# Optimization experiments

Hardware: AMD Instinct MI355X
Metric: run time of the kernel (lower is better)

Reference implementation:

```python
import jax, jax.numpy as jnp
import numpy as np

N_NODES = 100000
N_EDGES = 1600000
NFEAT = 512
HIDDEN = 128
NCLASS = 40


def setup_inputs() -> dict:
    key = jax.random.key(0)
    ks = jax.random.split(key, 8)
    x = jax.random.normal(ks[0], (N_NODES, NFEAT), dtype=jnp.float32)
    edge_src = jax.random.randint(ks[1], (N_EDGES,), 0, N_NODES, dtype=jnp.int32)
    edge_dst = jax.random.randint(ks[2], (N_EDGES,), 0, N_NODES, dtype=jnp.int32)
    # normalized adjacency values (D^-1/2 A D^-1/2 style), all positive
    edge_val = jax.random.uniform(ks[3], (N_EDGES,), dtype=jnp.float32)
    # glorot-ish init like pygcn's reset_parameters
    W1 = jax.random.normal(ks[4], (NFEAT, HIDDEN), dtype=jnp.float32) / np.sqrt(NFEAT)
    b1 = jnp.zeros((HIDDEN,), dtype=jnp.float32)
    W2 = jax.random.normal(ks[5], (HIDDEN, NCLASS), dtype=jnp.float32) / np.sqrt(HIDDEN)
    b2 = jnp.zeros((NCLASS,), dtype=jnp.float32)
    return {"x": x, "edge_src": edge_src, "edge_dst": edge_dst, "edge_val": edge_val,
            "W1": W1, "b1": b1, "W2": W2, "b2": b2}


def _gcn_layer(h, edge_src, edge_dst, edge_val, W, b):
    # support = h @ W ; out = spmm(adj, support) + b
    support = h @ W                                  # [N, d_out]
    msg = support[edge_src] * edge_val[:, None]      # [E, d_out] gather
    agg = jax.ops.segment_sum(msg, edge_dst, num_segments=N_NODES)  # scatter-add
    return agg + b


def reference(x, edge_src, edge_dst, edge_val, W1, b1, W2, b2):
    h = _gcn_layer(x, edge_src, edge_dst, edge_val, W1, b1)
    h = jax.nn.relu(h)
    # dropout=0.0 -> branch skipped (faithful to `if self.dropout:` with falsy value)
    h = _gcn_layer(h, edge_src, edge_dst, edge_val, W2, b2)
    return jax.nn.log_softmax(h, axis=1)
```

## Files before the change

kernel.cpp:

```cpp
#include <hip/hip_runtime.h>
#include <stdint.h>

#define NN 100000
#define NE 1600000
#define NF 512
#define NH 128
#define NC 40

typedef float f32x4 __attribute__((ext_vector_type(4)));
typedef short bf16x8 __attribute__((ext_vector_type(8)));

__device__ __forceinline__ unsigned short f2bf(float f){
    unsigned u = __float_as_uint(f);
    u = u + 0x7FFFu + ((u >> 16) & 1u);
    return (unsigned short)(u >> 16);
}
__device__ __forceinline__ unsigned pk2(float a, float b){
    return (unsigned)f2bf(a) | ((unsigned)f2bf(b) << 16);
}
__device__ __forceinline__ float bf2f(unsigned short s){
    return __uint_as_float(((unsigned)s) << 16);
}
__device__ __forceinline__ float blo(unsigned u){ return __uint_as_float(u << 16); }
__device__ __forceinline__ float bhi(unsigned u){ return __uint_as_float(u & 0xffff0000u); }

__global__ __launch_bounds__(256) void hist_prep(const int* __restrict__ edst,
                       int* __restrict__ deg, int* __restrict__ posw,
                       const float* __restrict__ W1, const float* __restrict__ W2,
                       unsigned short* __restrict__ W1t, unsigned short* __restrict__ W2t){
    if (blockIdx.x < 280){
        int tid = blockIdx.x * 256 + threadIdx.x;
        if (tid < NF * NH){
            int c = tid >> 9;
            int k = tid & 511;
            W1t[c * NF + k] = f2bf(W1[k * NH + c]);
        }
        int t2 = tid - NF * NH;
        if (t2 >= 0 && t2 < 48 * NH){
            int c = t2 >> 7;
            int k = t2 & 127;
            W2t[c * NH + k] = (c < NC) ? f2bf(W2[k * NC + c]) : (unsigned short)0;
        }
    } else {
        int tid = (blockIdx.x - 280) * 256 + threadIdx.x;
        if (tid < NE){
            int d = edst[tid];
            posw[tid] = atomicAdd(&deg[d], 1);
        }
    }
}

__global__ __launch_bounds__(256, 3) void gemm1(const float* __restrict__ x,
                                                const unsigned short* __restrict__ W1t,
                                                unsigned short* __restrict__ s1){
    __shared__ unsigned short Al[2][128 * 40];
    __shared__ unsigned short Bl[2][128 * 40];
    const int tid  = threadIdx.x;
    const int wid  = tid >> 6;
    const int lane = tid & 63;
    const int quad = lane >> 4;
    const int l15  = lane & 15;
    const int br   = blockIdx.x * 128;

    const int r    = tid >> 1;
    const int half = tid & 1;

    int arow = br + r; if (arow >= NN) arow = NN - 1;
    const float* aptr = x + (size_t)arow * NF + half * 16;
    const unsigned short* bptr = W1t + (size_t)r * NF + half * 16;

    float4 pa0, pa1, pa2, pa3;
    uint4  pb0, pb1;
    {
        const float4* ap = (const float4*)aptr;
        pa0 = ap[0]; pa1 = ap[1]; pa2 = ap[2]; pa3 = ap[3];
        const uint4* bp = (const uint4*)bptr;
        pb0 = bp[0]; pb1 = bp[1];
        unsigned* Ad = (unsigned*)&Al[0][r * 40 + half * 16];
        Ad[0] = pk2(pa0.x, pa0.y); Ad[1] = pk2(pa0.z, pa0.w);
        Ad[2] = pk2(pa1.x, pa1.y); Ad[3] = pk2(pa1.z, pa1.w);
        Ad[4] = pk2(pa2.x, pa2.y); Ad[5] = pk2(pa2.z, pa2.w);
        Ad[6] = pk2(pa3.x, pa3.y); Ad[7] = pk2(pa3.z, pa3.w);
        uint4* Bd = (uint4*)&Bl[0][r * 40 + half * 16];
        Bd[0] = pb0; Bd[1] = pb1;
    }
    __syncthreads();

    f32x4 acc[2][8];
#pragma unroll
    for (int i = 0; i < 2; i++)
#pragma unroll
        for (int j = 0; j < 8; j++) acc[i][j] = (f32x4){0.f, 0.f, 0.f, 0.f};

    int cur = 0;
    for (int ks = 0; ks < NF; ks += 32){
        const bool more = (ks + 32 < NF);
        if (more){
            const float4* ap = (const float4*)(aptr + ks + 32);
            pa0 = ap[0]; pa1 = ap[1]; pa2 = ap[2]; pa3 = ap[3];
            const uint4* bp = (const uint4*)(bptr + ks + 32);
            pb0 = bp[0]; pb1 = bp[1];
        }

        bf16x8 a0 = *(const bf16x8*)&Al[cur][(wid * 32 +      l15) * 40 + quad * 8];
        bf16x8 a1 = *(const bf16x8*)&Al[cur][(wid * 32 + 16 + l15) * 40 + quad * 8];
        bf16x8 bb[8];
#pragma unroll
        for (int ct = 0; ct < 8; ct++)
            bb[ct] = *(const bf16x8*)&Bl[cur][(ct * 16 + l15) * 40 + quad * 8];
#pragma unroll
        for (int ct = 0; ct < 8; ct++){
            acc[0][ct] = __builtin_amdgcn_mfma_f32_16x16x32_bf16(a0, bb[ct], acc[0][ct], 0, 0, 0);
            acc[1][ct] = __builtin_amdgcn_mfma_f32_16x16x32_bf16(a1, bb[ct], acc[1][ct], 0, 0, 0);
        }

        if (more){
            int nxt = cur ^ 1;
            unsigned* Ad = (unsigned*)&Al[nxt][r * 40 + half * 16];
            Ad[0] = pk2(pa0.x, pa0.y); Ad[1] = pk2(pa0.z, pa0.w);
            Ad[2] = pk2(pa1.x, pa1.y); Ad[3] = pk2(pa1.z, pa1.w);
            Ad[4] = pk2(pa2.x, pa2.y); Ad[5] = pk2(pa2.z, pa2.w);
            Ad[6] = pk2(pa3.x, pa3.y); Ad[7] = pk2(pa3.z, pa3.w);
            uint4* Bd = (uint4*)&Bl[nxt][r * 40 + half * 16];
            Bd[0] = pb0; Bd[1] = pb1;
        }
        __syncthreads();
        cur ^= 1;
    }

#pragma unroll
    for (int rt = 0; rt < 2; rt++)
#pragma unroll
        for (int ct = 0; ct < 8; ct++)
#pragma unroll
            for (int i = 0; i < 4; i++){
                int row = br + wid * 32 + rt * 16 + quad * 4 + i;
                if (row < NN) s1[(size_t)row * NH + ct * 16 + l15] = f2bf(acc[rt][ct][i]);
            }
}

__global__ void scan1(const int* __restrict__ deg, int* __restrict__ rs, int* __restrict__ bsums){
    __shared__ int sh[256];
    int t = threadIdx.x;
    int base = blockIdx.x * 1024 + t * 4;
    int v0 = (base     < NN) ? deg[base]     : 0;
    int v1 = (base + 1 < NN) ? deg[base + 1] : 0;
    int v2 = (base + 2 < NN) ? deg[base + 2] : 0;
    int v3 = (base + 3 < NN) ? deg[base + 3] : 0;
    int ssum = v0 + v1 + v2 + v3;
    sh[t] = ssum;
    __syncthreads();
    for (int o = 1; o < 256; o <<= 1){
        int tmp = (t >= o) ? sh[t - o] : 0;
        __syncthreads();
        sh[t] += tmp;
        __syncthreads();
    }
    int excl = sh[t] - ssum;
    if (base     < NN) rs[base]     = excl; excl += v0;
    if (base + 1 < NN) rs[base + 1] = excl; excl += v1;
    if (base + 2 < NN) rs[base + 2] = excl; excl += v2;
    if (base + 3 < NN) rs[base + 3] = excl;
    if (t == 255) bsums[blockIdx.x] = sh[255];
}

__global__ void scan3(int* __restrict__ rs, const int* __restrict__ bsums){
    __shared__ int add_s;
    int t = threadIdx.x;
    if (t < 64){
        int v = 0;
        if (t      < blockIdx.x) v  = bsums[t];
        if (t + 64 < blockIdx.x) v += bsums[t + 64];
#pragma unroll
        for (int o = 32; o; o >>= 1) v += __shfl_xor(v, o, 64);
        if (t == 0) add_s = v;
    }
    __syncthreads();
    int add = add_s;
    int base = blockIdx.x * 1024 + t * 4;
#pragma unroll
    for (int i = 0; i < 4; i++)
        if (base + i < NN) rs[base + i] += add;
}

__global__ __launch_bounds__(256) void scatter_k(const int* __restrict__ esrc, const int* __restrict__ edst,
                          const float* __restrict__ eval, const int* __restrict__ rs,
                          const int* __restrict__ posw, int2* __restrict__ pk){
    int tid = blockIdx.x * 256 + threadIdx.x;
    if (tid < NE){
        int d = edst[tid];
        int pos = rs[d] + posw[tid];
        pk[pos] = make_int2(esrc[tid], __float_as_int(eval[tid]));
    }
}

__global__ __launch_bounds__(256) void agg1(const uint2* __restrict__ s1v,
                                            const int* __restrict__ rs,
                                            const int2* __restrict__ pk,
                                            const float* __restrict__ b1, uint2* __restrict__ h){
    const int lane  = threadIdx.x & 63;
    const int half  = lane >> 5;
    const int hl    = lane & 31;
    const int lbase = half * 32;
    const int node  = blockIdx.x * 8 + (threadIdx.x >> 6) * 2 + half;

    int s = rs[node];
    int e = (node == NN - 1) ? NE : rs[node + 1];
    float a0 = 0.f, a1 = 0.f, a2 = 0.f, a3 = 0.f;

    for (int base = s; base < e; base += 32){
        int cnt = e - base; if (cnt > 32) cnt = 32;
        int2 rec = make_int2(0, 0);
        if (hl < cnt) rec = pk[base + hl];
        int j = 0;
        for (; j + 8 <= cnt; j += 8){
            int is[8];
#pragma unroll
            for (int q = 0; q < 8; q++) is[q] = __shfl(rec.x, lbase + j + q, 64);
            uint2 us[8];
#pragma unroll
            for (int q = 0; q < 8; q++) us[q] = s1v[(size_t)is[q] * 32 + hl];
            float vs[8];
#pragma unroll
            for (int q = 0; q < 8; q++) vs[q] = __int_as_float(__shfl(rec.y, lbase + j + q, 64));
#pragma unroll
            for (int q = 0; q < 8; q++){
                a0 += vs[q] * blo(us[q].x); a1 += vs[q] * bhi(us[q].x);
                a2 += vs[q] * blo(us[q].y); a3 += vs[q] * bhi(us[q].y);
            }
        }
        for (; j < cnt; j++){
            int   i0 = __shfl(rec.x, lbase + j, 64);
            float v0 = __int_as_float(__shfl(rec.y, lbase + j, 64));
            uint2 u  = s1v[(size_t)i0 * 32 + hl];
            a0 += v0 * blo(u.x); a1 += v0 * bhi(u.x);
            a2 += v0 * blo(u.y); a3 += v0 * bhi(u.y);
        }
    }
    a0 += b1[4 * hl];     a1 += b1[4 * hl + 1];
    a2 += b1[4 * hl + 2]; a3 += b1[4 * hl + 3];
    a0 = fmaxf(a0, 0.f); a1 = fmaxf(a1, 0.f);
    a2 = fmaxf(a2, 0.f); a3 = fmaxf(a3, 0.f);
    h[(size_t)node * 32 + hl] = make_uint2(pk2(a0, a1), pk2(a2, a3));
}

__global__ __launch_bounds__(256) void gemm2(const unsigned short* __restrict__ h,
                                             const unsigned short* __restrict__ W2t,
                                             unsigned short* __restrict__ s2p){
    const int tid  = threadIdx.x;
    const int wid  = tid >> 6;
    const int lane = tid & 63;
    const int quad = lane >> 4;
    const int l15  = lane & 15;
    const int row0 = blockIdx.x * 64 + wid * 16;

    bf16x8 bf[3][4];
#pragma unroll
    for (int ct = 0; ct < 3; ct++)
#pragma unroll
        for (int ks = 0; ks < 4; ks++)
            bf[ct][ks] = *(const bf16x8*)&W2t[(ct * 16 + l15) * NH + ks * 32 + quad * 8];

    int arow = row0 + l15; if (arow >= NN) arow = NN - 1;
    const unsigned short* ap = h + (size_t)arow * NH;

    bf16x8 a[4];
#pragma unroll
    for (int ks = 0; ks < 4; ks++) a[ks] = *(const bf16x8*)&ap[ks * 32 + quad * 8];

    f32x4 acc[3];
#pragma unroll
    for (int ct = 0; ct < 3; ct++) acc[ct] = (f32x4){0.f, 0.f, 0.f, 0.f};
#pragma unroll
    for (int ks = 0; ks < 4; ks++)
#pragma unroll
        for (int ct = 0; ct < 3; ct++)
            acc[ct] = __builtin_amdgcn_mfma_f32_16x16x32_bf16(a[ks], bf[ct][ks], acc[ct], 0, 0, 0);

#pragma unroll
    for (int ct = 0; ct < 3; ct++)
#pragma unroll
        for (int i = 0; i < 4; i++){
            int row = row0 + quad * 4 + i;
            if (row < NN) s2p[(size_t)row * 64 + ct * 16 + l15] = f2bf(acc[ct][i]);
        }
}

__global__ __launch_bounds__(256) void agg2(const unsigned* __restrict__ s2v,
                                            const int* __restrict__ rs,
                                            const int2* __restrict__ pk,
                                            const float* __restrict__ b2, float* __restrict__ out){
    const int lane  = threadIdx.x & 63;
    const int half  = lane >> 5;
    const int hl    = lane & 31;
    const int lbase = half * 32;
    const int node  = blockIdx.x * 8 + (threadIdx.x >> 6) * 2 + half;

    int s = rs[node];
    int e = (node == NN - 1) ? NE : rs[node + 1];
    float a0 = 0.f, a1 = 0.f;

    for (int base = s; base < e; base += 32){
        int cnt = e - base; if (cnt > 32) cnt = 32;
        int2 rec = make_int2(0, 0);
        if (hl < cnt) rec = pk[base + hl];
        int j = 0;
        for (; j + 8 <= cnt; j += 8){
            int is[8];
#pragma unroll
            for (int q = 0; q < 8; q++) is[q] = __shfl(rec.x, lbase + j + q, 64);
            unsigned us[8];
#pragma unroll
            for (int q = 0; q < 8; q++) us[q] = s2v[(size_t)is[q] * 32 + hl];
            float vs[8];
#pragma unroll
            for (int q = 0; q < 8; q++) vs[q] = __int_as_float(__shfl(rec.y, lbase + j + q, 64));
#pragma unroll
            for (int q = 0; q < 8; q++){
                a0 += vs[q] * blo(us[q]); a1 += vs[q] * bhi(us[q]);
            }
        }
        for (; j < cnt; j++){
            int   i0 = __shfl(rec.x, lbase + j, 64);
            float v0 = __int_as_float(__shfl(rec.y, lbase + j, 64));
            unsigned u = s2v[(size_t)i0 * 32 + hl];
            a0 += v0 * blo(u); a1 += v0 * bhi(u);
        }
    }
    bool act = hl < 20;
    float z0 = act ? (a0 + b2[2 * hl])     : -INFINITY;
    float z1 = act ? (a1 + b2[2 * hl + 1]) : -INFINITY;
    float m = fmaxf(z0, z1);
#pragma unroll
    for (int o = 16; o; o >>= 1) m = fmaxf(m, __shfl_xor(m, o, 64));
    float pe = act ? (__expf(z0 - m) + __expf(z1 - m)) : 0.f;
#pragma unroll
    for (int o = 16; o; o >>= 1) pe += __shfl_xor(pe, o, 64);
    if (act){
        float l = __logf(pe);
        float2 o2 = make_float2(z0 - m - l, z1 - m - l);
        *(float2*)(out + (size_t)node * NC + 2 * hl) = o2;
    }
}

extern "C" void kernel_launch(void* const* d_in, const int* in_sizes, int n_in,
                              void* d_out, int out_size, void* d_ws, size_t ws_size,
                              hipStream_t stream) {
    const float* x    = (const float*)d_in[0];
    const int*   esrc = (const int*)  d_in[1];
    const int*   edst = (const int*)  d_in[2];
    const float* eval = (const float*)d_in[3];
    const float* W1   = (const float*)d_in[4];
    const float* b1   = (const float*)d_in[5];
    const float* W2   = (const float*)d_in[6];
    const float* b2   = (const float*)d_in[7];
    float* out = (float*)d_out;

    char* ws = (char*)d_ws;
    size_t off = 0;
    auto alloc = [&](size_t bytes) -> void* {
        void* p = ws + off;
        off += (bytes + 255) & ~(size_t)255;
        return p;
    };
    unsigned short* W1t  = (unsigned short*)alloc((size_t)NF * NH * 2);
    unsigned short* W2t  = (unsigned short*)alloc((size_t)48 * NH * 2);
    unsigned short* s1   = (unsigned short*)alloc((size_t)NN * NH * 2);
    unsigned short* h    = (unsigned short*)alloc((size_t)NN * NH * 2);
    unsigned short* s2p  = (unsigned short*)alloc((size_t)NN * 64 * 2);
    int*   deg   = (int*)  alloc((size_t)NN * 4);
    int*   rs    = (int*)  alloc((size_t)NN * 4);
    int*   bsums = (int*)  alloc(128 * 4);
    int*   posw  = (int*)  alloc((size_t)NE * 4);
    int2*  pk    = (int2*) alloc((size_t)NE * 8);

    hipMemsetAsync(deg, 0, (size_t)NN * 4, stream);

    hist_prep<<<280 + (NE + 255) / 256, 256, 0, stream>>>(edst, deg, posw, W1, W2, W1t, W2t);
    gemm1    <<<(NN + 127) / 128, 256, 0, stream>>>(x, W1t, s1);
    scan1    <<<98, 256, 0, stream>>>(deg, rs, bsums);
    scan3    <<<98, 256, 0, stream>>>(rs, bsums);
    scatter_k<<<(NE + 255) / 256, 256, 0, stream>>>(esrc, edst, eval, rs, posw, pk);
    agg1     <<<NN / 8, 256, 0, stream>>>((const uint2*)s1, rs, pk, b1, (uint2*)h);
    gemm2    <<<(NN + 63) / 64, 256, 0, stream>>>(h, W2t, s2p);
    agg2     <<<NN / 8, 256, 0, stream>>>((const unsigned*)s2p, rs, pk, b2, out);
}
```

Before: 553.7 us.

## Widen SpMM gathers to 16-byte loads and pack more nodes per wavefront

```diff
diff --git a/kernel.cpp b/kernel.cpp
--- a/kernel.cpp
+++ b/kernel.cpp
@@ -17,9 +17,6 @@
 }
 __device__ __forceinline__ unsigned pk2(float a, float b){
     return (unsigned)f2bf(a) | ((unsigned)f2bf(b) << 16);
-}
-__device__ __forceinline__ float bf2f(unsigned short s){
-    return __uint_as_float(((unsigned)s) << 16);
 }
 __device__ __forceinline__ float blo(unsigned u){ return __uint_as_float(u << 16); }
 __device__ __forceinline__ float bhi(unsigned u){ return __uint_as_float(u & 0xffff0000u); }
@@ -194,54 +191,74 @@
     }
 }
 
-__global__ __launch_bounds__(256) void agg1(const uint2* __restrict__ s1v,
+__global__ __launch_bounds__(256) void agg1(const uint4* __restrict__ s1v,
                                             const int* __restrict__ rs,
                                             const int2* __restrict__ pk,
-                                            const float* __restrict__ b1, uint2* __restrict__ h){
+                                            const float* __restrict__ b1, uint4* __restrict__ h){
     const int lane  = threadIdx.x & 63;
-    const int half  = lane >> 5;
-    const int hl    = lane & 31;
-    const int lbase = half * 32;
-    const int node  = blockIdx.x * 8 + (threadIdx.x >> 6) * 2 + half;
-
-    int s = rs[node];
-    int e = (node == NN - 1) ? NE : rs[node + 1];
-    float a0 = 0.f, a1 = 0.f, a2 = 0.f, a3 = 0.f;
-
-    for (int base = s; base < e; base += 32){
-        int cnt = e - base; if (cnt > 32) cnt = 32;
-        int2 rec = make_int2(0, 0);
-        if (hl < cnt) rec = pk[base + hl];
+    const int quad  = lane >> 4;
+    const int hl    = lane & 15;
+    const int lbase = quad * 16;
+    const int node  = blockIdx.x * 16 + (threadIdx.x >> 6) * 4 + quad;
+
+    const int s = rs[node];
+    const int e = (node == NN - 1) ? NE : rs[node + 1];
+    float a[8];
+#pragma unroll
+    for (int t = 0; t < 8; t++) a[t] = 0.f;
+
+    int2 rec = make_int2(0, 0);
+    {
+        int c0 = e - s; if (c0 > 16) c0 = 16;
+        if (hl < c0) rec = pk[s + hl];
+    }
+    for (int base = s; base < e; base += 16){
+        int cnt = e - base; if (cnt > 16) cnt = 16;
+        int2 cur = rec;
+        int nb = base + 16;
+        if (nb < e){
+            int cn = e - nb; if (cn > 16) cn = 16;
+            rec = make_int2(0, 0);
+            if (hl < cn) rec = pk[nb + hl];
+        }
         int j = 0;
         for (; j + 8 <= cnt; j += 8){
             int is[8];
 #pragma unroll
-            for (int q = 0; q < 8; q++) is[q] = __shfl(rec.x, lbase + j + q, 64);
-            uint2 us[8];
-#pragma unroll
-            for (int q = 0; q < 8; q++) us[q] = s1v[(size_t)is[q] * 32 + hl];
+            for (int q = 0; q < 8; q++) is[q] = __shfl(cur.x, lbase + j + q, 64);
+            uint4 us[8];
+#pragma unroll
+            for (int q = 0; q < 8; q++) us[q] = s1v[(size_t)is[q] * 16 + hl];
             float vs[8];
 #pragma unroll
-            for (int q = 0; q < 8; q++) vs[q] = __int_as_float(__shfl(rec.y, lbase + j + q, 64));
+            for (int q = 0; q < 8; q++) vs[q] = __int_as_float(__shfl(cur.y, lbase + j + q, 64));
 #pragma unroll
             for (int q = 0; q < 8; q++){
-                a0 += vs[q] * blo(us[q].x); a1 += vs[q] * bhi(us[q].x);
-                a2 += vs[q] * blo(us[q].y); a3 += vs[q] * bhi(us[q].y);
+                float v = vs[q];
+                a[0] += v * blo(us[q].x); a[1] += v * bhi(us[q].x);
+                a[2] += v * blo(us[q].y); a[3] += v * bhi(us[q].y);
+                a[4] += v * blo(us[q].z); a[5] += v * bhi(us[q].z);
+                a[6] += v * blo(us[q].w); a[7] += v * bhi(us[q].w);
             }
         }
         for (; j < cnt; j++){
-            int   i0 = __shfl(rec.x, lbase + j, 64);
-            float v0 = __int_as_float(__shfl(rec.y, lbase + j, 64));
-            uint2 u  = s1v[(size_t)i0 * 32 + hl];
-            a0 += v0 * blo(u.x); a1 += v0 * bhi(u.x);
-            a2 += v0 * blo(u.y); a3 += v0 * bhi(u.y);
-        }
-    }
-    a0 += b1[4 * hl];     a1 += b1[4 * hl + 1];
-    a2 += b1[4 * hl + 2]; a3 += b1[4 * hl + 3];
-    a0 = fmaxf(a0, 0.f); a1 = fmaxf(a1, 0.f);
-    a2 = fmaxf(a2, 0.f); a3 = fmaxf(a3, 0.f);
-    h[(size_t)node * 32 + hl] = make_uint2(pk2(a0, a1), pk2(a2, a3));
+            int   i0 = __shfl(cur.x, lbase + j, 64);
+            float v0 = __int_as_float(__shfl(cur.y, lbase + j, 64));
+            uint4 u  = s1v[(size_t)i0 * 16 + hl];
+            a[0] += v0 * blo(u.x); a[1] += v0 * bhi(u.x);
+            a[2] += v0 * blo(u.y); a[3] += v0 * bhi(u.y);
+            a[4] += v0 * blo(u.z); a[5] += v0 * bhi(u.z);
+            a[6] += v0 * blo(u.w); a[7] += v0 * bhi(u.w);
+        }
+    }
+    const float4* b1v = (const float4*)b1;
+    float4 bA = b1v[2 * hl], bB = b1v[2 * hl + 1];
+    a[0] += bA.x; a[1] += bA.y; a[2] += bA.z; a[3] += bA.w;
+    a[4] += bB.x; a[5] += bB.y; a[6] += bB.z; a[7] += bB.w;
+#pragma unroll
+    for (int t = 0; t < 8; t++) a[t] = fmaxf(a[t], 0.f);
+    h[(size_t)node * 16 + hl] = make_uint4(pk2(a[0], a[1]), pk2(a[2], a[3]),
+                                           pk2(a[4], a[5]), pk2(a[6], a[7]));
 }
 
 __global__ __launch_bounds__(256) void gemm2(const unsigned short* __restrict__ h,
@@ -286,60 +303,94 @@
         }
 }
 
-__global__ __launch_bounds__(256) void agg2(const unsigned* __restrict__ s2v,
+__global__ __launch_bounds__(256) void agg2(const uint4* __restrict__ s2v,
                                             const int* __restrict__ rs,
                                             const int2* __restrict__ pk,
                                             const float* __restrict__ b2, float* __restrict__ out){
     const int lane  = threadIdx.x & 63;
-    const int half  = lane >> 5;
-    const int hl    = lane & 31;
-    const int lbase = half * 32;
-    const int node  = blockIdx.x * 8 + (threadIdx.x >> 6) * 2 + half;
-
-    int s = rs[node];
-    int e = (node == NN - 1) ? NE : rs[node + 1];
-    float a0 = 0.f, a1 = 0.f;
-
-    for (int base = s; base < e; base += 32){
-        int cnt = e - base; if (cnt > 32) cnt = 32;
-        int2 rec = make_int2(0, 0);
-        if (hl < cnt) rec = pk[base + hl];
-        int j = 0;
-        for (; j + 8 <= cnt; j += 8){
+    const int oct   = lane >> 3;
+    const int hl    = lane & 7;
+    const int lbase = oct * 8;
+    const int node  = blockIdx.x * 32 + (threadIdx.x >> 6) * 8 + oct;
+
+    const int s = rs[node];
+    const int e = (node == NN - 1) ? NE : rs[node + 1];
+    float a[8];
+#pragma unroll
+    for (int t = 0; t < 8; t++) a[t] = 0.f;
+
+    int2 rec = make_int2(0, 0);
+    {
+        int c0 = e - s; if (c0 > 8) c0 = 8;
+        if (hl < c0) rec = pk[s + hl];
+    }
+    for (int base = s; base < e; base += 8){
+        int cnt = e - base; if (cnt > 8) cnt = 8;
+        int2 cur = rec;
+        int nb = base + 8;
+        if (nb < e){
+            int cn = e - nb; if (cn > 8) cn = 8;
+            rec = make_int2(0, 0);
+            if (hl < cn) rec = pk[nb + hl];
+        }
+        if (cnt == 8){
             int is[8];
 #pragma unroll
-            for (int q = 0; q < 8; q++) is[q] = __shfl(rec.x, lbase + j + q, 64);
-            unsigned us[8];
-#pragma unroll
-            for (int q = 0; q < 8; q++) us[q] = s2v[(size_t)is[q] * 32 + hl];
+            for (int q = 0; q < 8; q++) is[q] = __shfl(cur.x, lbase + q, 64);
+            uint4 us[8];
+#pragma unroll
+            for (int q = 0; q < 8; q++) us[q] = s2v[(size_t)is[q] * 8 + hl];
             float vs[8];
 #pragma unroll
-            for (int q = 0; q < 8; q++) vs[q] = __int_as_float(__shfl(rec.y, lbase + j + q, 64));
+            for (int q = 0; q < 8; q++) vs[q] = __int_as_float(__shfl(cur.y, lbase + q, 64));
 #pragma unroll
             for (int q = 0; q < 8; q++){
-                a0 += vs[q] * blo(us[q]); a1 += vs[q] * bhi(us[q]);
+                float v = vs[q];
+                a[0] += v * blo(us[q].x); a[1] += v * bhi(us[q].x);
+                a[2] += v * blo(us[q].y); a[3] += v * bhi(us[q].y);
+                a[4] += v * blo(us[q].z); a[5] += v * bhi(us[q].z);
+                a[6] += v * blo(us[q].w); a[7] += v * bhi(us[q].w);
             }
-        }
-        for (; j < cnt; j++){
-            int   i0 = __shfl(rec.x, lbase + j, 64);
-            float v0 = __int_as_float(__shfl(rec.y, lbase + j, 64));
-            unsigned u = s2v[(size_t)i0 * 32 + hl];
-            a0 += v0 * blo(u); a1 += v0 * bhi(u);
-        }
-    }
-    bool act = hl < 20;
-    float z0 = act ? (a0 + b2[2 * hl])     : -INFINITY;
-    float z1 = act ? (a1 + b2[2 * hl + 1]) : -INFINITY;
-    float m = fmaxf(z0, z1);
-#pragma unroll
-    for (int o = 16; o; o >>= 1) m = fmaxf(m, __shfl_xor(m, o, 64));
-    float pe = act ? (__expf(z0 - m) + __expf(z1 - m)) : 0.f;
-#pragma unroll
-    for (int o = 16; o; o >>= 1) pe += __shfl_xor(pe, o, 64);
+        } else {
+            for (int j = 0; j < cnt; j++){
+                int   i0 = __shfl(cur.x, lbase + j, 64);
+                float v0 = __int_as_float(__shfl(cur.y, lbase + j, 64));
+                uint4 u  = s2v[(size_t)i0 * 8 + hl];
+                a[0] += v0 * blo(u.x); a[1] += v0 * bhi(u.x);
+                a[2] += v0 * blo(u.y); a[3] += v0 * bhi(u.y);
+                a[4] += v0 * blo(u.z); a[5] += v0 * bhi(u.z);
+                a[6] += v0 * blo(u.w); a[7] += v0 * bhi(u.w);
+            }
+        }
+    }
+    const bool act = hl < 5;
+    float z[8];
     if (act){
-        float l = __logf(pe);
-        float2 o2 = make_float2(z0 - m - l, z1 - m - l);
-        *(float2*)(out + (size_t)node * NC + 2 * hl) = o2;
+        const float4* b2v = (const float4*)b2;
+        float4 cA = b2v[2 * hl], cB = b2v[2 * hl + 1];
+        z[0] = a[0] + cA.x; z[1] = a[1] + cA.y; z[2] = a[2] + cA.z; z[3] = a[3] + cA.w;
+        z[4] = a[4] + cB.x; z[5] = a[5] + cB.y; z[6] = a[6] + cB.z; z[7] = a[7] + cB.w;
+    } else {
+#pragma unroll
+        for (int t = 0; t < 8; t++) z[t] = -INFINITY;
+    }
+    float m = z[0];
+#pragma unroll
+    for (int t = 1; t < 8; t++) m = fmaxf(m, z[t]);
+#pragma unroll
+    for (int o = 4; o; o >>= 1) m = fmaxf(m, __shfl_xor(m, o, 8));
+    float pe = 0.f;
+    if (act){
+#pragma unroll
+        for (int t = 0; t < 8; t++) pe += __expf(z[t] - m);
+    }
+#pragma unroll
+    for (int o = 4; o; o >>= 1) pe += __shfl_xor(pe, o, 8);
+    if (act){
+        float l = __logf(pe) + m;
+        float* op = out + (size_t)node * NC + 8 * hl;
+        *(float4*)op       = make_float4(z[0] - l, z[1] - l, z[2] - l, z[3] - l);
+        *(float4*)(op + 4) = make_float4(z[4] - l, z[5] - l, z[6] - l, z[7] - l);
     }
 }
 
@@ -381,7 +432,7 @@
     scan1    <<<98, 256, 0, stream>>>(deg, rs, bsums);
     scan3    <<<98, 256, 0, stream>>>(rs, bsums);
     scatter_k<<<(NE + 255) / 256, 256, 0, stream>>>(esrc, edst, eval, rs, posw, pk);
-    agg1     <<<NN / 8, 256, 0, stream>>>((const uint2*)s1, rs, pk, b1, (uint2*)h);
+    agg1     <<<NN / 16, 256, 0, stream>>>((const uint4*)s1, rs, pk, b1, (uint4*)h);
     gemm2    <<<(NN + 63) / 64, 256, 0, stream>>>(h, W2t, s2p);
-    agg2     <<<NN / 8, 256, 0, stream>>>((const unsigned*)s2p, rs, pk, b2, out);
-}
+    agg2     <<<NN / 32, 256, 0, stream>>>((const uint4*)s2p, rs, pk, b2, out);
+}
```

Result: no change. 554.7 us (+0.2%).
